# Performance work log

Measured on AMD Instinct MI355X. Metric: run time of the kernel, lower is better.

The kernel has to match this reference:

```python
import jax, jax.numpy as jnp
import numpy as np

N, E, D = 50000, 800000, 256
H1, C1 = 4, 64          # conv1: heads=4, out=64 -> concat dim 256
H2, C2 = 1, 2           # conv2: heads=1, out=2, concat=False
NEG_SLOPE = 0.2
LN_EPS = 1e-5


def _gatv2(x, src, dst, n, Wl, bl, Wr, br, att, bias, concat):
    """PyG GATv2Conv (eval mode, add_self_loops already applied to src/dst)."""
    H, C = att.shape
    xl = (x @ Wl + bl).reshape(n, H, C)   # source-side transform (x_j)
    xr = (x @ Wr + br).reshape(n, H, C)   # target-side transform (x_i)
    e = xl[src] + xr[dst]                 # [E, H, C]
    e = jnp.where(e > 0, e, NEG_SLOPE * e)          # LeakyReLU(0.2)
    logits = jnp.einsum('ehc,hc->eh', e, att)       # [E, H]
    m = jax.ops.segment_max(logits, dst, num_segments=n)
    a = jnp.exp(logits - m[dst])
    denom = jax.ops.segment_sum(a, dst, num_segments=n)
    alpha = a / denom[dst]                          # segment softmax over in-edges
    msg = xl[src] * alpha[:, :, None]               # [E, H, C]
    out = jax.ops.segment_sum(msg, dst, num_segments=n)  # [n, H, C]
    if concat:
        return out.reshape(n, H * C) + bias
    return out.mean(axis=1) + bias


def _layernorm(x, g, b):
    mu = x.mean(-1, keepdims=True)
    var = ((x - mu) ** 2).mean(-1, keepdims=True)
    return (x - mu) * jax.lax.rsqrt(var + LN_EPS) * g + b


def setup_inputs() -> dict:
    key = jax.random.key(0)
    ks = jax.random.split(key, 20)
    s = 0.05
    HC = H1 * C1
    return {
        'x': jax.random.normal(ks[0], (N, D), jnp.float32),
        'edge_index': jax.random.randint(ks[1], (2, E), 0, N, jnp.int64),
        # conv1 params
        'W1l': jax.random.normal(ks[2], (D, HC), jnp.float32) * s,
        'b1l': jnp.zeros((HC,), jnp.float32),
        'W1r': jax.random.normal(ks[3], (D, HC), jnp.float32) * s,
        'b1r': jnp.zeros((HC,), jnp.float32),
        'att1': jax.random.normal(ks[4], (H1, C1), jnp.float32) * s,
        'bias1': jnp.zeros((HC,), jnp.float32),
        # conv2 params (in = HC, out = 2, 1 head, concat=False)
        'W2l': jax.random.normal(ks[5], (HC, H2 * C2), jnp.float32) * s,
        'b2l': jnp.zeros((H2 * C2,), jnp.float32),
        'W2r': jax.random.normal(ks[6], (HC, H2 * C2), jnp.float32) * s,
        'b2r': jnp.zeros((H2 * C2,), jnp.float32),
        'att2': jax.random.normal(ks[7], (H2, C2), jnp.float32) * s,
        'bias2': jnp.zeros((C2,), jnp.float32),
        # skip Linear(D, HC)
        'Wskip': jax.random.normal(ks[8], (D, HC), jnp.float32) * s,
        'bskip': jnp.zeros((HC,), jnp.float32),
        # LayerNorm(HC)
        'gamma': jnp.ones((HC,), jnp.float32),
        'beta': jnp.zeros((HC,), jnp.float32),
    }


def reference(x, edge_index, W1l, b1l, W1r, b1r, att1, bias1,
              W2l, b2l, W2r, b2r, att2, bias2, Wskip, bskip, gamma, beta):
    n = x.shape[0]
    loops = jnp.arange(n, dtype=edge_index.dtype)  # PyG add_self_loops=True
    src = jnp.concatenate([edge_index[0], loops])
    dst = jnp.concatenate([edge_index[1], loops])
    h = _gatv2(x, src, dst, n, W1l, b1l, W1r, b1r, att1, bias1, True)
    h = h + x @ Wskip + bskip
    h = jax.nn.elu(_layernorm(h, gamma, beta))
    # dropout p=0.3 is identity in eval mode
    return _gatv2(h, src, dst, n, W2l, b2l, W2r, b2r, att2, bias2, False)
```

## Files before the change

### kernel.cpp

```cpp
#include <hip/hip_runtime.h>
#include <hip/hip_bf16.h>

#define NNODES 50000
#define NEDGES 800000
#define CAP    80
#define CAST_BLKS 12500
#define TR_BLKS   192
#define ZERO_BLKS 196

using bf16 = __hip_bfloat16;
using short8 = __attribute__((ext_vector_type(8))) short;
using float4v = __attribute__((ext_vector_type(4))) float;

__device__ __forceinline__ float us2f(unsigned short u) {
    union { unsigned int i; float f; } c; c.i = ((unsigned int)u) << 16; return c.f;
}
__device__ __forceinline__ float scrub(float v) {
    if (!(v == v)) return 0.f;
    return fminf(fmaxf(v, -1e30f), 1e30f);
}

__global__ __launch_bounds__(256) void prep_k(
    const float* __restrict__ x, bf16* __restrict__ xb,
    const float* __restrict__ W0, const float* __restrict__ W1,
    const float* __restrict__ W2,
    bf16* __restrict__ T0, bf16* __restrict__ T1, bf16* __restrict__ T2,
    int* __restrict__ deg)
{
    __shared__ float tile[32][33];
    int b = blockIdx.x;
    if (b < CAST_BLKS) {
        size_t i = (size_t)b * 256 + threadIdx.x;
        float4 v = ((const float4*)x)[i];
        bf16 o[4] = {__float2bfloat16(v.x), __float2bfloat16(v.y),
                     __float2bfloat16(v.z), __float2bfloat16(v.w)};
        *(uint2*)(xb + 4 * i) = *(uint2*)o;
        return;
    }
    b -= CAST_BLKS;
    if (b < TR_BLKS) {
        int bz = b >> 6, rem = b & 63;
        int bx = rem & 7, by = rem >> 3;
        const float* W = (bz == 0) ? W0 : (bz == 1) ? W1 : W2;
        bf16*       T  = (bz == 0) ? T0 : (bz == 1) ? T1 : T2;
        const int r0 = by * 32, c0 = bx * 32;
        const int tc = threadIdx.x & 31, tr = threadIdx.x >> 5;
#pragma unroll
        for (int i = 0; i < 4; i++)
            tile[tr + 8 * i][tc] = W[(size_t)(r0 + tr + 8 * i) * 256 + c0 + tc];
        __syncthreads();
#pragma unroll
        for (int i = 0; i < 4; i++)
            T[(size_t)(c0 + tr + 8 * i) * 256 + r0 + tc] =
                __float2bfloat16(tile[tc][tr + 8 * i]);
        return;
    }
    b -= TR_BLKS;
    int i = b * 256 + threadIdx.x;
    if (i < NNODES) deg[i] = 0;
}

__global__ __launch_bounds__(256) void gemm3(
    const bf16* __restrict__ A,
    const bf16* __restrict__ Bt0, const bf16* __restrict__ Bt1,
    const bf16* __restrict__ Bt2,
    const float* __restrict__ bias0, const float* __restrict__ bias1,
    const float* __restrict__ bias2, const float* __restrict__ bias2b,
    bf16* __restrict__ o0, bf16* __restrict__ o1, bf16* __restrict__ o2, int M)
{
    __shared__ bf16 As[128 * 40];
    __shared__ bf16 Bs0[64 * 40], Bs1[64 * 40], Bs2[64 * 40];
    const int t = threadIdx.x;
    const int lane = t & 63, w = t >> 6;
    const int quad = lane >> 4, r16 = lane & 15;
    const int m0 = blockIdx.x * 128, n0 = blockIdx.y * 64;
    const int arow = t >> 1, acol = (t & 1) * 16;
    const int brow = t >> 2, bcol = (t & 3) * 8;

    float4v acc[3][4][2];
#pragma unroll
    for (int j = 0; j < 3; j++)
#pragma unroll
        for (int tt = 0; tt < 4; tt++)
#pragma unroll
            for (int mf = 0; mf < 2; mf++)
                acc[j][tt][mf] = (float4v){0.f, 0.f, 0.f, 0.f};

    for (int k0 = 0; k0 < 256; k0 += 32) {
        int gm = m0 + arow; if (gm >= M) gm = M - 1;
        const bf16* ap = A + (size_t)gm * 256 + k0 + acol;
        *(uint4*)(As + arow * 40 + acol)     = *(const uint4*)(ap);
        *(uint4*)(As + arow * 40 + acol + 8) = *(const uint4*)(ap + 8);
        const size_t bo = (size_t)(n0 + brow) * 256 + k0 + bcol;
        *(uint4*)(Bs0 + brow * 40 + bcol) = *(const uint4*)(Bt0 + bo);
        *(uint4*)(Bs1 + brow * 40 + bcol) = *(const uint4*)(Bt1 + bo);
        *(uint4*)(Bs2 + brow * 40 + bcol) = *(const uint4*)(Bt2 + bo);
        __syncthreads();
        short8 a0 = *(const short8*)(As + (w * 32 + r16) * 40 + quad * 8);
        short8 a1 = *(const short8*)(As + (w * 32 + 16 + r16) * 40 + quad * 8);
#pragma unroll
        for (int tt = 0; tt < 4; tt++) {
            const int boff = (tt * 16 + r16) * 40 + quad * 8;
            short8 b0 = *(const short8*)(Bs0 + boff);
            acc[0][tt][0] = __builtin_amdgcn_mfma_f32_16x16x32_bf16(a0, b0, acc[0][tt][0], 0, 0, 0);
            acc[0][tt][1] = __builtin_amdgcn_mfma_f32_16x16x32_bf16(a1, b0, acc[0][tt][1], 0, 0, 0);
            short8 b1 = *(const short8*)(Bs1 + boff);
            acc[1][tt][0] = __builtin_amdgcn_mfma_f32_16x16x32_bf16(a0, b1, acc[1][tt][0], 0, 0, 0);
            acc[1][tt][1] = __builtin_amdgcn_mfma_f32_16x16x32_bf16(a1, b1, acc[1][tt][1], 0, 0, 0);
            short8 b2 = *(const short8*)(Bs2 + boff);
            acc[2][tt][0] = __builtin_amdgcn_mfma_f32_16x16x32_bf16(a0, b2, acc[2][tt][0], 0, 0, 0);
            acc[2][tt][1] = __builtin_amdgcn_mfma_f32_16x16x32_bf16(a1, b2, acc[2][tt][1], 0, 0, 0);
        }
        __syncthreads();
    }
#pragma unroll
    for (int tt = 0; tt < 4; tt++) {
        int n = n0 + tt * 16 + r16;
        float bv0 = bias0[n], bv1 = bias1[n], bv2 = bias2[n] + bias2b[n];
#pragma unroll
        for (int mf = 0; mf < 2; mf++) {
#pragma unroll
            for (int j = 0; j < 4; j++) {
                int m = m0 + w * 32 + mf * 16 + quad * 4 + j;
                if (m < M) {
                    size_t idx = (size_t)m * 256 + n;
                    o0[idx] = __float2bfloat16(acc[0][tt][mf][j] + bv0);
                    o1[idx] = __float2bfloat16(acc[1][tt][mf][j] + bv1);
                    o2[idx] = __float2bfloat16(acc[2][tt][mf][j] + bv2);
                }
            }
        }
    }
}

__global__ void scatter_pad(const int* __restrict__ ei,
                            int* __restrict__ deg, int* __restrict__ csr) {
    __shared__ int stS;
    if (threadIdx.x == 0) {
        int orv = 0;
#pragma unroll
        for (int k = 1; k < 32; k += 2) orv |= ei[k];
        stS = orv ? 1 : 2;
    }
    __syncthreads();
    int st = stS;
    int e = blockIdx.x * 256 + threadIdx.x;
    if (e >= NEDGES) return;
    int s = ei[(size_t)st * e];
    int d = ei[(size_t)st * (NEDGES + e)];
    if ((unsigned)s >= NNODES) s = 0;
    if ((unsigned)d >= NNODES) d = 0;
    int pos = atomicAdd(&deg[d], 1);
    if (pos < CAP) csr[(size_t)d * CAP + pos] = s;
}

__global__ __launch_bounds__(256) void node_conv1(
    const int* __restrict__ deg, const int* __restrict__ csr,
    const bf16* __restrict__ xl, const bf16* __restrict__ xr_,
    const bf16* __restrict__ acc_,
    const float* __restrict__ att,
    const float* __restrict__ g_, const float* __restrict__ bt_,
    const float* __restrict__ W2l, const float* __restrict__ b2l,
    const float* __restrict__ W2r, const float* __restrict__ b2r,
    float* __restrict__ xl2, float* __restrict__ xr2)
{
    const int node = blockIdx.x * 4 + (threadIdx.x >> 6);
    if (node >= NNODES) return;
    const int lane = threadIdx.x & 63;
    const int ch0 = (lane >> 4) * 64 + (lane & 15) * 4;

    const float4 att4 = *(const float4*)(att + ch0);
    ushort4 xru = *(const ushort4*)(xr_ + (size_t)node * 256 + ch0);
    const float4 xr4 = {us2f(xru.x), us2f(xru.y), us2f(xru.z), us2f(xru.w)};

    const char* __restrict__ xlB = (const char*)xl;
    const unsigned offL = (unsigned)(ch0 * 2);
#define ROW(srcv) (*(const ushort4*)(xlB + (size_t)((((unsigned)(srcv)) << 9) + offL)))

    float s = 0.f, a0 = 0.f, a1 = 0.f, a2 = 0.f, a3 = 0.f;

#define EDGE1(r, valid)                                                        \
    {                                                                          \
        float v0 = us2f((r).x), v1 = us2f((r).y),                              \
              v2 = us2f((r).z), v3 = us2f((r).w);                              \
        float e0 = v0 + xr4.x; e0 = fmaxf(e0, 0.2f * e0);                      \
        float e1 = v1 + xr4.y; e1 = fmaxf(e1, 0.2f * e1);                      \
        float e2 = v2 + xr4.z; e2 = fmaxf(e2, 0.2f * e2);                      \
        float e3 = v3 + xr4.w; e3 = fmaxf(e3, 0.2f * e3);                      \
        float part = att4.x * e0 + att4.y * e1 + att4.z * e2 + att4.w * e3;    \
        part += __shfl_xor(part, 1);                                           \
        part += __shfl_xor(part, 2);                                           \
        part += __shfl_xor(part, 4);                                           \
        part += __shfl_xor(part, 8);                                           \
        float lg = fminf(fmaxf(part, -60.f), 60.f);                            \
        float pe = __expf(lg);                                                 \
        pe = (valid) ? pe : 0.f;                                               \
        s += pe;                                                               \
        a0 = fmaf(pe, v0, a0); a1 = fmaf(pe, v1, a1);                          \
        a2 = fmaf(pe, v2, a2); a3 = fmaf(pe, v3, a3);                          \
    }

    { ushort4 rs = ROW(node); EDGE1(rs, true); }

    int dg = deg[node]; if (dg > CAP) dg = CAP;
    const int* __restrict__ q = csr + (size_t)node * CAP;

    int i0 = q[0]; if ((unsigned)i0 >= NNODES) i0 = 0;
    int i1 = q[1]; if ((unsigned)i1 >= NNODES) i1 = 0;
    int i2 = q[2]; if ((unsigned)i2 >= NNODES) i2 = 0;
    int i3 = q[3]; if ((unsigned)i3 >= NNODES) i3 = 0;
    ushort4 r0 = ROW(i0), r1 = ROW(i1), r2 = ROW(i2), r3 = ROW(i3);

    for (int p = 0; p < dg; p += 4) {
        int j0 = q[p + 4]; if ((unsigned)j0 >= NNODES) j0 = 0;
        int j1 = q[p + 5]; if ((unsigned)j1 >= NNODES) j1 = 0;
        int j2 = q[p + 6]; if ((unsigned)j2 >= NNODES) j2 = 0;
        int j3 = q[p + 7]; if ((unsigned)j3 >= NNODES) j3 = 0;
        ushort4 rn0 = ROW(j0), rn1 = ROW(j1), rn2 = ROW(j2), rn3 = ROW(j3);

        EDGE1(r0, true);
        EDGE1(r1, (p + 1) < dg);
        EDGE1(r2, (p + 2) < dg);
        EDGE1(r3, (p + 3) < dg);

        r0 = rn0; r1 = rn1; r2 = rn2; r3 = rn3;
    }
#undef EDGE1
#undef ROW

    float D = s;
    if (!(D > 0.f)) D = 1.f;
    ushort4 acu = *(const ushort4*)(acc_ + (size_t)node * 256 + ch0);
    float t0 = scrub(us2f(acu.x) + a0 / D);
    float t1 = scrub(us2f(acu.y) + a1 / D);
    float t2 = scrub(us2f(acu.z) + a2 / D);
    float t3 = scrub(us2f(acu.w) + a3 / D);

    float s1 = t0 + t1 + t2 + t3;
    float s2 = t0 * t0 + t1 * t1 + t2 * t2 + t3 * t3;
#pragma unroll
    for (int o = 32; o > 0; o >>= 1) { s1 += __shfl_xor(s1, o); s2 += __shfl_xor(s2, o); }
    float mu  = s1 * (1.f / 256.f);
    float var = fmaxf(s2 * (1.f / 256.f) - mu * mu, 0.f);
    float rstd = rsqrtf(var + 1e-5f);
    const float4 g4 = *(const float4*)(g_ + ch0);
    const float4 b4 = *(const float4*)(bt_ + ch0);
    float y0 = (t0 - mu) * rstd * g4.x + b4.x;
    float y1 = (t1 - mu) * rstd * g4.y + b4.y;
    float y2 = (t2 - mu) * rstd * g4.z + b4.z;
    float y3 = (t3 - mu) * rstd * g4.w + b4.w;
    float h0 = y0 > 0.f ? y0 : (__expf(y0) - 1.f);
    float h1 = y1 > 0.f ? y1 : (__expf(y1) - 1.f);
    float h2 = y2 > 0.f ? y2 : (__expf(y2) - 1.f);
    float h3 = y3 > 0.f ? y3 : (__expf(y3) - 1.f);

    const float4 wla = *(const float4*)(W2l + ch0 * 2);
    const float4 wlb = *(const float4*)(W2l + ch0 * 2 + 4);
    const float4 wra = *(const float4*)(W2r + ch0 * 2);
    const float4 wrb = *(const float4*)(W2r + ch0 * 2 + 4);
    float p0 = h0 * wla.x + h1 * wla.z + h2 * wlb.x + h3 * wlb.z;
    float p1 = h0 * wla.y + h1 * wla.w + h2 * wlb.y + h3 * wlb.w;
    float p2 = h0 * wra.x + h1 * wra.z + h2 * wrb.x + h3 * wrb.z;
    float p3 = h0 * wra.y + h1 * wra.w + h2 * wrb.y + h3 * wrb.w;
#pragma unroll
    for (int o = 32; o > 0; o >>= 1) {
        p0 += __shfl_xor(p0, o); p1 += __shfl_xor(p1, o);
        p2 += __shfl_xor(p2, o); p3 += __shfl_xor(p3, o);
    }
    if (lane == 0) {
        xl2[(size_t)node * 2 + 0] = scrub(p0 + b2l[0]);
        xl2[(size_t)node * 2 + 1] = scrub(p1 + b2l[1]);
        xr2[(size_t)node * 2 + 0] = scrub(p2 + b2r[0]);
        xr2[(size_t)node * 2 + 1] = scrub(p3 + b2r[1]);
    }
}

__global__ __launch_bounds__(256) void node_conv2(
    const int* __restrict__ deg, const int* __restrict__ csr,
    const float* __restrict__ xl2, const float* __restrict__ xr2,
    const float* __restrict__ att2, const float* __restrict__ bias2,
    float* __restrict__ out)
{
    int node = blockIdx.x * 8 + (threadIdx.x >> 5);
    if (node >= NNODES) return;
    int hl = threadIdx.x & 31;
    float a0 = att2[0], a1 = att2[1];
    float2 xr = *(const float2*)(xr2 + (size_t)node * 2);
    int dg = deg[node]; if (dg > CAP) dg = CAP;
    const int* __restrict__ q = csr + (size_t)node * CAP;

    float s = 0.f, o0 = 0.f, o1 = 0.f;
    {
        float2 v = *(const float2*)(xl2 + (size_t)node * 2);
        float e0 = v.x + xr.x; e0 = fmaxf(e0, 0.2f * e0);
        float e1 = v.y + xr.y; e1 = fmaxf(e1, 0.2f * e1);
        float lg = fminf(fmaxf(a0 * e0 + a1 * e1, -60.f), 60.f);
        float pe = (hl == 0) ? __expf(lg) : 0.f;
        s = pe; o0 = pe * v.x; o1 = pe * v.y;
    }
    for (int pb = 0; pb < dg; pb += 32) {
        int p = pb + hl;
        bool valid = p < dg;
        int src = q[p];
        if ((unsigned)src >= NNODES) src = 0;
        float2 v = *(const float2*)(xl2 + (size_t)src * 2);
        float e0 = v.x + xr.x; e0 = fmaxf(e0, 0.2f * e0);
        float e1 = v.y + xr.y; e1 = fmaxf(e1, 0.2f * e1);
        float lg = fminf(fmaxf(a0 * e0 + a1 * e1, -60.f), 60.f);
        float pe = valid ? __expf(lg) : 0.f;
        s += pe; o0 = fmaf(pe, v.x, o0); o1 = fmaf(pe, v.y, o1);
    }
#pragma unroll
    for (int o = 16; o > 0; o >>= 1) {
        s += __shfl_xor(s, o); o0 += __shfl_xor(o0, o); o1 += __shfl_xor(o1, o);
    }
    if (hl == 0) {
        if (!(s > 0.f)) { s = 1.f; o0 = 0.f; o1 = 0.f; }
        float inv = 1.f / s;
        out[(size_t)node * 2 + 0] = scrub(o0 * inv + bias2[0]);
        out[(size_t)node * 2 + 1] = scrub(o1 * inv + bias2[1]);
    }
}

extern "C" void kernel_launch(void* const* d_in, const int* in_sizes, int n_in,
                              void* d_out, int out_size, void* d_ws, size_t ws_size,
                              hipStream_t stream) {
    const float* x     = (const float*)d_in[0];
    const int*   ei    = (const int*)d_in[1];
    const float* W1l   = (const float*)d_in[2];
    const float* b1l   = (const float*)d_in[3];
    const float* W1r   = (const float*)d_in[4];
    const float* b1r   = (const float*)d_in[5];
    const float* att1  = (const float*)d_in[6];
    const float* bias1 = (const float*)d_in[7];
    const float* W2l   = (const float*)d_in[8];
    const float* b2l   = (const float*)d_in[9];
    const float* W2r   = (const float*)d_in[10];
    const float* b2r   = (const float*)d_in[11];
    const float* att2  = (const float*)d_in[12];
    const float* bias2 = (const float*)d_in[13];
    const float* Wsk   = (const float*)d_in[14];
    const float* bsk   = (const float*)d_in[15];
    const float* g_    = (const float*)d_in[16];
    const float* bt_   = (const float*)d_in[17];

    size_t off = 0;
    auto alloc = [&](size_t b) {
        void* p = (char*)d_ws + off;
        off += (b + 255) & ~(size_t)255;
        return p;
    };
    int*   deg  = (int*)alloc((size_t)NNODES * 4);
    int*   csr  = (int*)alloc(((size_t)NNODES * CAP + 256) * 4);
    float* xl2  = (float*)alloc((size_t)NNODES * 8);
    float* xr2  = (float*)alloc((size_t)NNODES * 8);
    bf16*  Wt1l = (bf16*)alloc(256 * 256 * 2);
    bf16*  Wt1r = (bf16*)alloc(256 * 256 * 2);
    bf16*  Wtsk = (bf16*)alloc(256 * 256 * 2);
    bf16*  xb   = (bf16*)alloc((size_t)NNODES * 256 * 2);
    bf16*  xl1  = (bf16*)alloc((size_t)NNODES * 256 * 2);
    bf16*  xr1  = (bf16*)alloc((size_t)NNODES * 256 * 2);
    bf16*  acc1 = (bf16*)alloc((size_t)NNODES * 256 * 2);

    prep_k<<<CAST_BLKS + TR_BLKS + ZERO_BLKS, 256, 0, stream>>>(
        x, xb, W1l, W1r, Wsk, Wt1l, Wt1r, Wtsk, deg);

    gemm3<<<dim3((NNODES + 127) / 128, 4), 256, 0, stream>>>(
        xb, Wt1l, Wt1r, Wtsk, b1l, b1r, bsk, bias1, xl1, xr1, acc1, NNODES);

    scatter_pad<<<(NEDGES + 255) / 256, 256, 0, stream>>>(ei, deg, csr);

    node_conv1<<<(NNODES + 3) / 4, 256, 0, stream>>>(deg, csr, xl1, xr1, acc1,
                                                     att1, g_, bt_, W2l, b2l, W2r, b2r,
                                                     xl2, xr2);
    node_conv2<<<(NNODES + 7) / 8, 256, 0, stream>>>(deg, csr, xl2, xr2, att2, bias2,
                                                     (float*)d_out);
}
```

Before: 334.4 us.

## Split conv1 edge loop across half-waves with 8-channel lanes; shrink GEMM M-tile

The node_conv1 aggregation now has each lane cover 8 channels with 16-byte gathers. The two half-waves process alternating edges (self loop first), and their partial sums are merged with a cross-half shuffle before LayerNorm. This halves the serial edge-loop length per node and widens each gather, which targets the latency-bound neighbor gather. Separately, the fused 3-output GEMM drops from 128-row to 64-row tiles to launch more blocks, at the cost of reloading B tiles more often.

```diff
diff --git a/kernel.cpp b/kernel.cpp
--- a/kernel.cpp
+++ b/kernel.cpp
@@ -10,6 +10,7 @@
 
 using bf16 = __hip_bfloat16;
 using short8 = __attribute__((ext_vector_type(8))) short;
+using ushort8v = __attribute__((ext_vector_type(8))) unsigned short;
 using float4v = __attribute__((ext_vector_type(4))) float;
 
 __device__ __forceinline__ float us2f(unsigned short u) {
@@ -68,48 +69,40 @@
     const float* __restrict__ bias2, const float* __restrict__ bias2b,
     bf16* __restrict__ o0, bf16* __restrict__ o1, bf16* __restrict__ o2, int M)
 {
-    __shared__ bf16 As[128 * 40];
+    __shared__ bf16 As[64 * 40];
     __shared__ bf16 Bs0[64 * 40], Bs1[64 * 40], Bs2[64 * 40];
     const int t = threadIdx.x;
     const int lane = t & 63, w = t >> 6;
     const int quad = lane >> 4, r16 = lane & 15;
-    const int m0 = blockIdx.x * 128, n0 = blockIdx.y * 64;
-    const int arow = t >> 1, acol = (t & 1) * 16;
-    const int brow = t >> 2, bcol = (t & 3) * 8;
-
-    float4v acc[3][4][2];
+    const int m0 = blockIdx.x * 64, n0 = blockIdx.y * 64;
+    const int lrow = t >> 2, lk = (t & 3) * 8;
+
+    float4v acc[3][4];
 #pragma unroll
     for (int j = 0; j < 3; j++)
 #pragma unroll
-        for (int tt = 0; tt < 4; tt++)
-#pragma unroll
-            for (int mf = 0; mf < 2; mf++)
-                acc[j][tt][mf] = (float4v){0.f, 0.f, 0.f, 0.f};
+        for (int i = 0; i < 4; i++) acc[j][i] = (float4v){0.f, 0.f, 0.f, 0.f};
 
     for (int k0 = 0; k0 < 256; k0 += 32) {
-        int gm = m0 + arow; if (gm >= M) gm = M - 1;
-        const bf16* ap = A + (size_t)gm * 256 + k0 + acol;
-        *(uint4*)(As + arow * 40 + acol)     = *(const uint4*)(ap);
-        *(uint4*)(As + arow * 40 + acol + 8) = *(const uint4*)(ap + 8);
-        const size_t bo = (size_t)(n0 + brow) * 256 + k0 + bcol;
-        *(uint4*)(Bs0 + brow * 40 + bcol) = *(const uint4*)(Bt0 + bo);
-        *(uint4*)(Bs1 + brow * 40 + bcol) = *(const uint4*)(Bt1 + bo);
-        *(uint4*)(Bs2 + brow * 40 + bcol) = *(const uint4*)(Bt2 + bo);
+        uint4 av = {0u, 0u, 0u, 0u};
+        int gm = m0 + lrow;
+        if (gm < M) av = *(const uint4*)(A + (size_t)gm * 256 + k0 + lk);
+        *(uint4*)(As + lrow * 40 + lk) = av;
+        const size_t bo = (size_t)(n0 + lrow) * 256 + k0 + lk;
+        *(uint4*)(Bs0 + lrow * 40 + lk) = *(const uint4*)(Bt0 + bo);
+        *(uint4*)(Bs1 + lrow * 40 + lk) = *(const uint4*)(Bt1 + bo);
+        *(uint4*)(Bs2 + lrow * 40 + lk) = *(const uint4*)(Bt2 + bo);
         __syncthreads();
-        short8 a0 = *(const short8*)(As + (w * 32 + r16) * 40 + quad * 8);
-        short8 a1 = *(const short8*)(As + (w * 32 + 16 + r16) * 40 + quad * 8);
+        short8 a = *(const short8*)(As + (w * 16 + r16) * 40 + quad * 8);
 #pragma unroll
         for (int tt = 0; tt < 4; tt++) {
             const int boff = (tt * 16 + r16) * 40 + quad * 8;
-            short8 b0 = *(const short8*)(Bs0 + boff);
-            acc[0][tt][0] = __builtin_amdgcn_mfma_f32_16x16x32_bf16(a0, b0, acc[0][tt][0], 0, 0, 0);
-            acc[0][tt][1] = __builtin_amdgcn_mfma_f32_16x16x32_bf16(a1, b0, acc[0][tt][1], 0, 0, 0);
-            short8 b1 = *(const short8*)(Bs1 + boff);
-            acc[1][tt][0] = __builtin_amdgcn_mfma_f32_16x16x32_bf16(a0, b1, acc[1][tt][0], 0, 0, 0);
-            acc[1][tt][1] = __builtin_amdgcn_mfma_f32_16x16x32_bf16(a1, b1, acc[1][tt][1], 0, 0, 0);
-            short8 b2 = *(const short8*)(Bs2 + boff);
-            acc[2][tt][0] = __builtin_amdgcn_mfma_f32_16x16x32_bf16(a0, b2, acc[2][tt][0], 0, 0, 0);
-            acc[2][tt][1] = __builtin_amdgcn_mfma_f32_16x16x32_bf16(a1, b2, acc[2][tt][1], 0, 0, 0);
+            short8 b0v = *(const short8*)(Bs0 + boff);
+            acc[0][tt] = __builtin_amdgcn_mfma_f32_16x16x32_bf16(a, b0v, acc[0][tt], 0, 0, 0);
+            short8 b1v = *(const short8*)(Bs1 + boff);
+            acc[1][tt] = __builtin_amdgcn_mfma_f32_16x16x32_bf16(a, b1v, acc[1][tt], 0, 0, 0);
+            short8 b2v = *(const short8*)(Bs2 + boff);
+            acc[2][tt] = __builtin_amdgcn_mfma_f32_16x16x32_bf16(a, b2v, acc[2][tt], 0, 0, 0);
         }
         __syncthreads();
     }
@@ -118,16 +111,13 @@
         int n = n0 + tt * 16 + r16;
         float bv0 = bias0[n], bv1 = bias1[n], bv2 = bias2[n] + bias2b[n];
 #pragma unroll
-        for (int mf = 0; mf < 2; mf++) {
-#pragma unroll
-            for (int j = 0; j < 4; j++) {
-                int m = m0 + w * 32 + mf * 16 + quad * 4 + j;
-                if (m < M) {
-                    size_t idx = (size_t)m * 256 + n;
-                    o0[idx] = __float2bfloat16(acc[0][tt][mf][j] + bv0);
-                    o1[idx] = __float2bfloat16(acc[1][tt][mf][j] + bv1);
-                    o2[idx] = __float2bfloat16(acc[2][tt][mf][j] + bv2);
-                }
+        for (int j = 0; j < 4; j++) {
+            int m = m0 + w * 16 + quad * 4 + j;
+            if (m < M) {
+                size_t idx = (size_t)m * 256 + n;
+                o0[idx] = __float2bfloat16(acc[0][tt][j] + bv0);
+                o1[idx] = __float2bfloat16(acc[1][tt][j] + bv1);
+                o2[idx] = __float2bfloat16(acc[2][tt][j] + bv2);
             }
         }
     }
@@ -167,103 +157,134 @@
     const int node = blockIdx.x * 4 + (threadIdx.x >> 6);
     if (node >= NNODES) return;
     const int lane = threadIdx.x & 63;
-    const int ch0 = (lane >> 4) * 64 + (lane & 15) * 4;
-
-    const float4 att4 = *(const float4*)(att + ch0);
-    ushort4 xru = *(const ushort4*)(xr_ + (size_t)node * 256 + ch0);
-    const float4 xr4 = {us2f(xru.x), us2f(xru.y), us2f(xru.z), us2f(xru.w)};
+    const int sub = lane >> 5;
+    const int ch0 = ((lane & 31) >> 3) * 64 + (lane & 7) * 8;
+
+    float attv[8], xrv[8];
+    {
+        const float4 aA = *(const float4*)(att + ch0);
+        const float4 aB = *(const float4*)(att + ch0 + 4);
+        attv[0]=aA.x; attv[1]=aA.y; attv[2]=aA.z; attv[3]=aA.w;
+        attv[4]=aB.x; attv[5]=aB.y; attv[6]=aB.z; attv[7]=aB.w;
+        ushort8v xu = *(const ushort8v*)((const unsigned short*)xr_ + (size_t)node * 256 + ch0);
+#pragma unroll
+        for (int i = 0; i < 8; i++) xrv[i] = us2f(xu[i]);
+    }
 
     const char* __restrict__ xlB = (const char*)xl;
     const unsigned offL = (unsigned)(ch0 * 2);
-#define ROW(srcv) (*(const ushort4*)(xlB + (size_t)((((unsigned)(srcv)) << 9) + offL)))
-
-    float s = 0.f, a0 = 0.f, a1 = 0.f, a2 = 0.f, a3 = 0.f;
-
-#define EDGE1(r, valid)                                                        \
-    {                                                                          \
-        float v0 = us2f((r).x), v1 = us2f((r).y),                              \
-              v2 = us2f((r).z), v3 = us2f((r).w);                              \
-        float e0 = v0 + xr4.x; e0 = fmaxf(e0, 0.2f * e0);                      \
-        float e1 = v1 + xr4.y; e1 = fmaxf(e1, 0.2f * e1);                      \
-        float e2 = v2 + xr4.z; e2 = fmaxf(e2, 0.2f * e2);                      \
-        float e3 = v3 + xr4.w; e3 = fmaxf(e3, 0.2f * e3);                      \
-        float part = att4.x * e0 + att4.y * e1 + att4.z * e2 + att4.w * e3;    \
-        part += __shfl_xor(part, 1);                                           \
-        part += __shfl_xor(part, 2);                                           \
-        part += __shfl_xor(part, 4);                                           \
-        part += __shfl_xor(part, 8);                                           \
-        float lg = fminf(fmaxf(part, -60.f), 60.f);                            \
-        float pe = __expf(lg);                                                 \
-        pe = (valid) ? pe : 0.f;                                               \
-        s += pe;                                                               \
-        a0 = fmaf(pe, v0, a0); a1 = fmaf(pe, v1, a1);                          \
-        a2 = fmaf(pe, v2, a2); a3 = fmaf(pe, v3, a3);                          \
-    }
-
-    { ushort4 rs = ROW(node); EDGE1(rs, true); }
+#define ROW8(srcv) (*(const ushort8v*)(xlB + (size_t)((((unsigned)(srcv)) << 9) + offL)))
 
     int dg = deg[node]; if (dg > CAP) dg = CAP;
     const int* __restrict__ q = csr + (size_t)node * CAP;
 
-    int i0 = q[0]; if ((unsigned)i0 >= NNODES) i0 = 0;
-    int i1 = q[1]; if ((unsigned)i1 >= NNODES) i1 = 0;
-    int i2 = q[2]; if ((unsigned)i2 >= NNODES) i2 = 0;
-    int i3 = q[3]; if ((unsigned)i3 >= NNODES) i3 = 0;
-    ushort4 r0 = ROW(i0), r1 = ROW(i1), r2 = ROW(i2), r3 = ROW(i3);
-
-    for (int p = 0; p < dg; p += 4) {
-        int j0 = q[p + 4]; if ((unsigned)j0 >= NNODES) j0 = 0;
-        int j1 = q[p + 5]; if ((unsigned)j1 >= NNODES) j1 = 0;
-        int j2 = q[p + 6]; if ((unsigned)j2 >= NNODES) j2 = 0;
-        int j3 = q[p + 7]; if ((unsigned)j3 >= NNODES) j3 = 0;
-        ushort4 rn0 = ROW(j0), rn1 = ROW(j1), rn2 = ROW(j2), rn3 = ROW(j3);
-
-        EDGE1(r0, true);
-        EDGE1(r1, (p + 1) < dg);
-        EDGE1(r2, (p + 2) < dg);
-        EDGE1(r3, (p + 3) < dg);
-
-        r0 = rn0; r1 = rn1; r2 = rn2; r3 = rn3;
-    }
-#undef EDGE1
-#undef ROW
+    float s = 0.f;
+    float a[8];
+#pragma unroll
+    for (int i = 0; i < 8; i++) a[i] = 0.f;
+
+    int e0 = sub;
+    int sv;
+    {
+        int qi = e0 - 1; if (qi < 0) qi = 0;
+        sv = q[qi];
+        if (e0 == 0) sv = node;
+        if ((unsigned)sv >= NNODES) sv = 0;
+    }
+    bool val = (e0 <= dg);
+    ushort8v row = ROW8(sv);
+
+    const int npair = (dg + 2) >> 1;
+    for (int k = 0; k < npair; k++) {
+        int en = e0 + 2;
+        int sn = q[en - 1];
+        if ((unsigned)sn >= NNODES) sn = 0;
+        ushort8v rown = ROW8(sn);
+        bool valn = (en <= dg);
+
+        float v[8];
+#pragma unroll
+        for (int i = 0; i < 8; i++) v[i] = us2f(row[i]);
+        float part = 0.f;
+#pragma unroll
+        for (int i = 0; i < 8; i++) {
+            float e = v[i] + xrv[i];
+            e = fmaxf(e, 0.2f * e);
+            part = fmaf(attv[i], e, part);
+        }
+        part += __shfl_xor(part, 1);
+        part += __shfl_xor(part, 2);
+        part += __shfl_xor(part, 4);
+        float lg = fminf(fmaxf(part, -60.f), 60.f);
+        float pe = __expf(lg);
+        pe = val ? pe : 0.f;
+        s += pe;
+#pragma unroll
+        for (int i = 0; i < 8; i++) a[i] = fmaf(pe, v[i], a[i]);
+
+        row = rown; val = valn; e0 = en;
+    }
+#undef ROW8
+
+    s += __shfl_xor(s, 32);
+#pragma unroll
+    for (int i = 0; i < 8; i++) a[i] += __shfl_xor(a[i], 32);
 
     float D = s;
     if (!(D > 0.f)) D = 1.f;
-    ushort4 acu = *(const ushort4*)(acc_ + (size_t)node * 256 + ch0);
-    float t0 = scrub(us2f(acu.x) + a0 / D);
-    float t1 = scrub(us2f(acu.y) + a1 / D);
-    float t2 = scrub(us2f(acu.z) + a2 / D);
-    float t3 = scrub(us2f(acu.w) + a3 / D);
-
-    float s1 = t0 + t1 + t2 + t3;
-    float s2 = t0 * t0 + t1 * t1 + t2 * t2 + t3 * t3;
-#pragma unroll
-    for (int o = 32; o > 0; o >>= 1) { s1 += __shfl_xor(s1, o); s2 += __shfl_xor(s2, o); }
+    float invD = 1.f / D;
+
+    float tot[8];
+    {
+        ushort8v au = *(const ushort8v*)((const unsigned short*)acc_ + (size_t)node * 256 + ch0);
+#pragma unroll
+        for (int i = 0; i < 8; i++) tot[i] = scrub(us2f(au[i]) + a[i] * invD);
+    }
+
+    float s1 = 0.f, s2 = 0.f;
+#pragma unroll
+    for (int i = 0; i < 8; i++) { s1 += tot[i]; s2 = fmaf(tot[i], tot[i], s2); }
+#pragma unroll
+    for (int o = 16; o > 0; o >>= 1) { s1 += __shfl_xor(s1, o); s2 += __shfl_xor(s2, o); }
     float mu  = s1 * (1.f / 256.f);
     float var = fmaxf(s2 * (1.f / 256.f) - mu * mu, 0.f);
     float rstd = rsqrtf(var + 1e-5f);
-    const float4 g4 = *(const float4*)(g_ + ch0);
-    const float4 b4 = *(const float4*)(bt_ + ch0);
-    float y0 = (t0 - mu) * rstd * g4.x + b4.x;
-    float y1 = (t1 - mu) * rstd * g4.y + b4.y;
-    float y2 = (t2 - mu) * rstd * g4.z + b4.z;
-    float y3 = (t3 - mu) * rstd * g4.w + b4.w;
-    float h0 = y0 > 0.f ? y0 : (__expf(y0) - 1.f);
-    float h1 = y1 > 0.f ? y1 : (__expf(y1) - 1.f);
-    float h2 = y2 > 0.f ? y2 : (__expf(y2) - 1.f);
-    float h3 = y3 > 0.f ? y3 : (__expf(y3) - 1.f);
-
-    const float4 wla = *(const float4*)(W2l + ch0 * 2);
-    const float4 wlb = *(const float4*)(W2l + ch0 * 2 + 4);
-    const float4 wra = *(const float4*)(W2r + ch0 * 2);
-    const float4 wrb = *(const float4*)(W2r + ch0 * 2 + 4);
-    float p0 = h0 * wla.x + h1 * wla.z + h2 * wlb.x + h3 * wlb.z;
-    float p1 = h0 * wla.y + h1 * wla.w + h2 * wlb.y + h3 * wlb.w;
-    float p2 = h0 * wra.x + h1 * wra.z + h2 * wrb.x + h3 * wrb.z;
-    float p3 = h0 * wra.y + h1 * wra.w + h2 * wrb.y + h3 * wrb.w;
-#pragma unroll
-    for (int o = 32; o > 0; o >>= 1) {
+
+    float gv[8], bv[8];
+    {
+        const float4 gA = *(const float4*)(g_ + ch0);
+        const float4 gB = *(const float4*)(g_ + ch0 + 4);
+        const float4 bA = *(const float4*)(bt_ + ch0);
+        const float4 bB = *(const float4*)(bt_ + ch0 + 4);
+        gv[0]=gA.x; gv[1]=gA.y; gv[2]=gA.z; gv[3]=gA.w;
+        gv[4]=gB.x; gv[5]=gB.y; gv[6]=gB.z; gv[7]=gB.w;
+        bv[0]=bA.x; bv[1]=bA.y; bv[2]=bA.z; bv[3]=bA.w;
+        bv[4]=bB.x; bv[5]=bB.y; bv[6]=bB.z; bv[7]=bB.w;
+    }
+    float h[8];
+#pragma unroll
+    for (int i = 0; i < 8; i++) {
+        float y = (tot[i] - mu) * rstd * gv[i] + bv[i];
+        h[i] = y > 0.f ? y : (__expf(y) - 1.f);
+        h[i] = scrub(h[i]);
+    }
+
+    float p0 = 0.f, p1 = 0.f, p2 = 0.f, p3 = 0.f;
+    {
+        const float4* wl = (const float4*)(W2l + ch0 * 2);
+        const float4* wr = (const float4*)(W2r + ch0 * 2);
+#pragma unroll
+        for (int i = 0; i < 4; i++) {
+            float4 wlv = wl[i];
+            float4 wrv = wr[i];
+            p0 = fmaf(h[2*i], wlv.x, p0); p0 = fmaf(h[2*i+1], wlv.z, p0);
+            p1 = fmaf(h[2*i], wlv.y, p1); p1 = fmaf(h[2*i+1], wlv.w, p1);
+            p2 = fmaf(h[2*i], wrv.x, p2); p2 = fmaf(h[2*i+1], wrv.z, p2);
+            p3 = fmaf(h[2*i], wrv.y, p3); p3 = fmaf(h[2*i+1], wrv.w, p3);
+        }
+    }
+#pragma unroll
+    for (int o = 16; o > 0; o >>= 1) {
         p0 += __shfl_xor(p0, o); p1 += __shfl_xor(p1, o);
         p2 += __shfl_xor(p2, o); p3 += __shfl_xor(p3, o);
     }
@@ -365,7 +386,7 @@
     prep_k<<<CAST_BLKS + TR_BLKS + ZERO_BLKS, 256, 0, stream>>>(
         x, xb, W1l, W1r, Wsk, Wt1l, Wt1r, Wtsk, deg);
 
-    gemm3<<<dim3((NNODES + 127) / 128, 4), 256, 0, stream>>>(
+    gemm3<<<dim3((NNODES + 63) / 64, 4), 256, 0, stream>>>(
         xb, Wt1l, Wt1r, Wtsk, b1l, b1r, bsk, bias1, xl1, xr1, acc1, NNODES);
 
     scatter_pad<<<(NEDGES + 255) / 256, 256, 0, stream>>>(ei, deg, csr);
```

Result: faster. 309.8 us (-7.4%).
